# Kernel tuning notes

Hardware: AMD Instinct MI355X
Metric: run time of the kernel (lower is better)

The kernel has to match this reference:

```python
import jax, jax.numpy as jnp
import numpy as np

B, T, D, H = 2, 2048, 1024, 16
HD = D // H
EPS = 1e-5


def setup_inputs() -> dict:
    key = jax.random.key(0)
    ks = jax.random.split(key, 6)
    scale = 0.02
    return {
        "x": jax.random.normal(ks[0], (B, T, D), dtype=jnp.float32),
        "wq": jax.random.normal(ks[1], (D, D), dtype=jnp.float32) * scale,
        "bq": jnp.zeros((D,), dtype=jnp.float32),
        "wk": jax.random.normal(ks[2], (D, D), dtype=jnp.float32) * scale,
        "bk": jnp.zeros((D,), dtype=jnp.float32),
        "wv": jax.random.normal(ks[3], (D, D), dtype=jnp.float32) * scale,
        "bv": jnp.zeros((D,), dtype=jnp.float32),
        "wg": jax.random.normal(ks[4], (D, D), dtype=jnp.float32) * scale,
        "bg": jnp.zeros((D,), dtype=jnp.float32),
        "gamma": jnp.ones((D,), dtype=jnp.float32),
        "beta": jnp.zeros((D,), dtype=jnp.float32),
    }


def reference(x, wq, bq, wk, bk, wv, bv, wg, bg, gamma, beta):
    b, t, d = x.shape
    # projections (torch Linear: y = x @ W^T + b, W stored as (out, in))
    def proj(w, bias):
        return jnp.einsum('btd,ed->bte', x, w) + bias
    q = proj(wq, bq).reshape(b, t, H, HD).swapaxes(1, 2)  # b h t hd
    k = proj(wk, bk).reshape(b, t, H, HD).swapaxes(1, 2)
    v = proj(wv, bv).reshape(b, t, H, HD).swapaxes(1, 2)
    # full (non-causal) attention as in the source
    scores = jnp.einsum('bhqd,bhkd->bhqk', q, k) / jnp.sqrt(jnp.float32(HD))
    attn = jax.nn.softmax(scores, axis=-1)
    out = jnp.einsum('bhqk,bhkd->bhqd', attn, v)
    out = out.swapaxes(1, 2).reshape(b, t, d)  # b t (h hd)
    gate = proj(wg, bg)
    y = gate * out
    # GroupNorm with n_heads groups over the channel (d_model) dim, per token
    yg = y.reshape(b, t, H, HD)
    mu = jnp.mean(yg, axis=-1, keepdims=True)
    var = jnp.var(yg, axis=-1, keepdims=True)
    yn = (yg - mu) / jnp.sqrt(var + EPS)
    yn = yn * gamma.reshape(H, HD) + beta.reshape(H, HD)
    return yn.reshape(b, t, d)
```

## Files before the change

kernel.cpp:

```cpp
#include <hip/hip_runtime.h>
#include <hip/hip_bf16.h>
#include <math.h>

namespace {
constexpr int kB = 2, kT = 2048, kD = 1024, kH = 16, kHD = 64;
}

typedef __attribute__((ext_vector_type(8))) short short8;
typedef __attribute__((ext_vector_type(4))) float f32x4;
typedef __attribute__((ext_vector_type(16))) float f32x16;

#if __has_builtin(__builtin_amdgcn_exp2f)
#define EXP2F(x) __builtin_amdgcn_exp2f(x)
#else
#define EXP2F(x) __expf((x) * 0.6931471805599453f)
#endif

__device__ __forceinline__ ushort f2bf(float f) {
  union { float f; uint u; } c; c.f = f;
  uint u = c.u + 0x7FFFu + ((c.u >> 16) & 1u);
  return (ushort)(u >> 16);
}

__device__ __forceinline__ float bf2f(ushort u) {
  union { uint u; float f; } c; c.u = ((uint)u) << 16; return c.f;
}

__device__ __forceinline__ uint pack_bf2(float a, float b) {
  uint r;
  asm("v_cvt_pk_bf16_f32 %0, %1, %2" : "=v"(r) : "v"(a), "v"(b));
  return r;
}

__device__ __forceinline__ void gload_lds16(const void* g, void* l) {
  __builtin_amdgcn_global_load_lds(
      (const __attribute__((address_space(1))) void*)g,
      (__attribute__((address_space(3))) void*)l, 16, 0, 0);
}

__global__ __launch_bounds__(256) void cvt_kernel(
    const float* __restrict__ x, const float* __restrict__ w0,
    const float* __restrict__ w1, const float* __restrict__ w2,
    const float* __restrict__ w3, ushort* __restrict__ out)
{
  const size_t g = (size_t)blockIdx.x * 256 + threadIdx.x;
  const size_t e = g * 4;
  const float* src; size_t rel;
  if (e < ((size_t)1 << 22)) { src = x; rel = e; }
  else {
    size_t e2 = e - ((size_t)1 << 22);
    int wi = (int)(e2 >> 20);
    src = wi == 0 ? w0 : wi == 1 ? w1 : wi == 2 ? w2 : w3;
    rel = e2 & (((size_t)1 << 20) - 1);
  }
  float4 v = *reinterpret_cast<const float4*>(src + rel);
  ushort4 u;
  u.x = f2bf(v.x); u.y = f2bf(v.y); u.z = f2bf(v.z); u.w = f2bf(v.w);
  *reinterpret_cast<ushort4*>(out + e) = u;
}

__device__ __forceinline__ void stage_half(
    const ushort* __restrict__ src, int row0, int kcol0,
    ushort* ldsbase, int wid, int lane)
{
#pragma unroll
  for (int part = 0; part < 2; ++part) {
    const int c = part * 512 + wid * 64 + lane;
    const int x = c * 16;
    const int o = x ^ (((x >> 7) & 3) << 4);
    const int r = o >> 6;
    const int cb = (o & 63) >> 1;
    gload_lds16(src + (size_t)(row0 + r) * kD + kcol0 + cb, ldsbase + (x >> 1));
  }
}

__device__ __forceinline__ short8 read_frag(const ushort* half, int r, int lg) {
  const int slot = lg ^ ((r >> 1) & 3);
  return *reinterpret_cast<const short8*>(&half[r * 32 + slot * 8]);
}

#define PH_BAR() do { asm volatile("" ::: "memory"); \
  __builtin_amdgcn_s_barrier(); asm volatile("" ::: "memory"); } while (0)

__global__ __launch_bounds__(512, 2) void proj_mfma_kernel(
    const ushort* __restrict__ Xb, const ushort* __restrict__ Wb,
    const float* __restrict__ bq, const float* __restrict__ bk,
    const float* __restrict__ bv, const float* __restrict__ bg,
    ushort* __restrict__ qo, ushort* __restrict__ ko,
    ushort* __restrict__ vt, ushort* __restrict__ go)
{
  const int mat = blockIdx.z;
  const ushort* Wm = Wb + (size_t)mat * 1024 * 1024;
  const float* bias = mat == 0 ? bq : mat == 1 ? bk : mat == 2 ? bv : bg;
  const int m0 = blockIdx.x * 256;
  const int n0g = blockIdx.y * 256;
  const int tid = threadIdx.x;
  const int wid = tid >> 6, lane = tid & 63;
  const int wr = wid >> 2, wc = wid & 3;
  const int wrow = wr * 128, wcol = wc * 64;
  const int lr = lane & 15, lg = lane >> 4;

  __shared__ ushort lds[65536];

  f32x4 acc[8][4];
#pragma unroll
  for (int i = 0; i < 8; ++i)
#pragma unroll
    for (int j = 0; j < 4; ++j) acc[i][j] = (f32x4){0.f, 0.f, 0.f, 0.f};

  short8 bfr[4];

#define STAGE_A(bu, h, kt) stage_half(Xb, m0,  (kt) * 64 + (h) * 32, \
    &lds[(bu) * 32768 + (h) * 8192], wid, lane)
#define STAGE_B(bu, h, kt) stage_half(Wm, n0g, (kt) * 64 + (h) * 32, \
    &lds[(bu) * 32768 + 16384 + (h) * 8192], wid, lane)

#define PHASE(bu, h, MB, READB, STAGE_STMT, DOVM)                          \
  {                                                                        \
    const ushort* Ah = &lds[(bu) * 32768 + (h) * 8192];                    \
    const ushort* Bh = &lds[(bu) * 32768 + 16384 + (h) * 8192];            \
    short8 af[4];                                                          \
    af[0] = read_frag(Ah, wrow + (MB + 0) * 16 + lr, lg);                  \
    af[1] = read_frag(Ah, wrow + (MB + 1) * 16 + lr, lg);                  \
    af[2] = read_frag(Ah, wrow + (MB + 2) * 16 + lr, lg);                  \
    af[3] = read_frag(Ah, wrow + (MB + 3) * 16 + lr, lg);                  \
    if (READB) {                                                           \
      bfr[0] = read_frag(Bh, wcol + 0 * 16 + lr, lg);                      \
      bfr[1] = read_frag(Bh, wcol + 1 * 16 + lr, lg);                      \
      bfr[2] = read_frag(Bh, wcol + 2 * 16 + lr, lg);                      \
      bfr[3] = read_frag(Bh, wcol + 3 * 16 + lr, lg);                      \
    }                                                                      \
    STAGE_STMT;                                                            \
    PH_BAR();                                                              \
    __builtin_amdgcn_s_setprio(1);                                         \
    _Pragma("unroll")                                                      \
    for (int m2 = 0; m2 < 4; ++m2)                                         \
      _Pragma("unroll")                                                    \
      for (int ni = 0; ni < 4; ++ni)                                       \
        acc[(MB) + m2][ni] = __builtin_amdgcn_mfma_f32_16x16x32_bf16(      \
            af[m2], bfr[ni], acc[(MB) + m2][ni], 0, 0, 0);                 \
    __builtin_amdgcn_s_setprio(0);                                         \
    if (DOVM) asm volatile("s_waitcnt vmcnt(4)" ::: "memory");             \
    PH_BAR();                                                              \
  }

  STAGE_A(0, 0, 0); STAGE_B(0, 0, 0);
  STAGE_A(0, 1, 0); STAGE_B(0, 1, 0);
  STAGE_A(1, 0, 1); STAGE_B(1, 0, 1);
  asm volatile("s_waitcnt vmcnt(4)" ::: "memory");
  PH_BAR();

#pragma unroll 1
  for (int it = 0; it < 8; ++it) {
    const int ta = 2 * it, tb = 2 * it + 1;
    const int tn0 = (ta + 2) & 15;
    const int tn1 = (tb + 2) & 15;
    PHASE(0, 0, 0, 1, (STAGE_A(1, 1, tb)),  0)
    PHASE(0, 0, 4, 0, (STAGE_B(1, 1, tb)),  0)
    PHASE(0, 1, 0, 1, (STAGE_A(0, 0, tn0)), 0)
    PHASE(0, 1, 4, 0, (STAGE_B(0, 0, tn0)), 1)
    PHASE(1, 0, 0, 1, (STAGE_A(0, 1, tn0)), 0)
    PHASE(1, 0, 4, 0, (STAGE_B(0, 1, tn0)), 0)
    PHASE(1, 1, 0, 1, (STAGE_A(1, 0, tn1)), 0)
    PHASE(1, 1, 4, 0, (STAGE_B(1, 0, tn1)), 1)
  }

#undef PHASE
#undef STAGE_A
#undef STAGE_B

  const float vsc = (mat == 0) ? 0.18033688f : 1.0f;

#pragma unroll
  for (int mi = 0; mi < 8; ++mi) {
    const int mbase = m0 + wrow + mi * 16 + 4 * lg;
    const int b = mbase >> 11, t0r = mbase & (kT - 1);
#pragma unroll
    for (int ni = 0; ni < 4; ++ni) {
      const int n = n0g + wcol + ni * 16 + lr;
      const float bn = bias[n];
      if (mat == 3) {
#pragma unroll
        for (int r = 0; r < 4; ++r)
          go[(size_t)(mbase + r) * kD + n] = f2bf(acc[mi][ni][r] + bn);
      } else if (mat == 2) {
        const int h = n >> 6, hd = n & 63;
        const int bh = b * kH + h;
        const int nh = hd >> 5, lv = hd & 31;
        const int kc = t0r >> 5, kk0 = t0r & 31;
        const int jf = kk0 >> 4, hi2 = (kk0 >> 3) & 1, jj0 = kk0 & 7;
        const int lane2 = lv + hi2 * 32;
        const size_t off =
            (((((size_t)bh * 64 + kc) * 2 + nh) * 2 + jf) * 64 + lane2) * 8 + jj0;
        ushort4 u;
        u.x = f2bf(acc[mi][ni][0] + bn); u.y = f2bf(acc[mi][ni][1] + bn);
        u.z = f2bf(acc[mi][ni][2] + bn); u.w = f2bf(acc[mi][ni][3] + bn);
        *reinterpret_cast<ushort4*>(&vt[off]) = u;
      } else {
        const int h = n >> 6, hd = n & 63;
        const int bh = b * kH + h;
        const int hk = hd >> 4, hi2 = (hd >> 3) & 1, jj = hd & 7;
        ushort* dst = (mat == 0) ? qo : ko;
#pragma unroll
        for (int r = 0; r < 4; ++r) {
          const int t = t0r + r;
          const int kc = t >> 5, kk = t & 31;
          const size_t off =
              ((((size_t)bh * 64 + kc) * 4 + hk) * 64 + kk + hi2 * 32) * 8 + jj;
          dst[off] = f2bf((acc[mi][ni][r] + bn) * vsc);
        }
      }
    }
  }
}

__global__ __launch_bounds__(256, 4) void attn_mfma32_kernel(
    const ushort* __restrict__ Qf, const ushort* __restrict__ Kf,
    const ushort* __restrict__ Vf, ushort* __restrict__ Op,
    float* __restrict__ lsumP)
{
  const int bid = blockIdx.x;
  const int xcd = bid & 7;
  const int j = bid >> 3;
  const int bh = xcd * 4 + (j >> 6);
  const int rem = j & 63;
  const int qt = rem & 15;
  const int ks = rem >> 4;
  const int tid = threadIdx.x, w = tid >> 6, lane = tid & 63;
  const int lq = lane & 31;
  const int hi = lane >> 5;

  const ushort* qfp = Qf + (((size_t)bh * 64 + (qt * 4 + w)) * 4) * 512;
  short8 aq[4];
#pragma unroll
  for (int hk = 0; hk < 4; ++hk)
    aq[hk] = *reinterpret_cast<const short8*>(&qfp[((size_t)hk * 64 + lane) * 8]);

  f32x16 oacc[2];
#pragma unroll
  for (int nh = 0; nh < 2; ++nh)
#pragma unroll
    for (int r = 0; r < 16; ++r) oacc[nh][r] = 0.f;
  float lsum = 0.f;

  const ushort* kfp = Kf + ((size_t)bh * 64 + ks * 16) * 2048;
  const ushort* vfp = Vf + ((size_t)bh * 64 + ks * 16) * 2048;

  for (int kt = 0; kt < 16; ++kt) {
    short8 kf_[4];
#pragma unroll
    for (int hk = 0; hk < 4; ++hk)
      kf_[hk] = *reinterpret_cast<const short8*>(&kfp[((size_t)hk * 64 + lane) * 8]);
    kfp += 2048;

    short8 vf[2][2];
#pragma unroll
    for (int nh = 0; nh < 2; ++nh)
#pragma unroll
      for (int jf = 0; jf < 2; ++jf)
        vf[nh][jf] = *reinterpret_cast<const short8*>(
            &vfp[(((size_t)nh * 2 + jf) * 64 + lane) * 8]);
    vfp += 2048;

    f32x16 s;
#pragma unroll
    for (int r = 0; r < 16; ++r) s[r] = 0.f;
    __builtin_amdgcn_s_setprio(1);
#pragma unroll
    for (int hk = 0; hk < 4; ++hk)
      s = __builtin_amdgcn_mfma_f32_32x32x16_bf16(kf_[hk], aq[hk], s, 0, 0, 0);
    __builtin_amdgcn_s_setprio(0);

    float p[16];
#pragma unroll
    for (int r = 0; r < 16; ++r) p[r] = EXP2F(s[r]);
    float t0 = 0.f, t1 = 0.f;
#pragma unroll
    for (int r = 0; r < 16; r += 2) { t0 += p[r]; t1 += p[r + 1]; }
    lsum += t0 + t1;

    uint pk[8];
#pragma unroll
    for (int m = 0; m < 8; ++m) pk[m] = pack_bf2(p[2 * m], p[2 * m + 1]);

    union { uint u[4]; short8 s8; } fa0, fa1;
#if __has_builtin(__builtin_amdgcn_permlane32_swap)
    {
      auto s0 = __builtin_amdgcn_permlane32_swap(pk[0], pk[2], false, false);
      auto s1 = __builtin_amdgcn_permlane32_swap(pk[1], pk[3], false, false);
      auto s2 = __builtin_amdgcn_permlane32_swap(pk[4], pk[6], false, false);
      auto s3 = __builtin_amdgcn_permlane32_swap(pk[5], pk[7], false, false);
      fa0.u[0] = s0[0]; fa0.u[2] = s0[1];
      fa0.u[1] = s1[0]; fa0.u[3] = s1[1];
      fa1.u[0] = s2[0]; fa1.u[2] = s2[1];
      fa1.u[1] = s3[0]; fa1.u[3] = s3[1];
    }
#else
    {
      const uint x0 = hi ? pk[0] : pk[2];
      const uint x1 = hi ? pk[1] : pk[3];
      const uint x2 = hi ? pk[4] : pk[6];
      const uint x3 = hi ? pk[5] : pk[7];
      const uint r0 = __shfl_xor((int)x0, 32);
      const uint r1 = __shfl_xor((int)x1, 32);
      const uint r2 = __shfl_xor((int)x2, 32);
      const uint r3 = __shfl_xor((int)x3, 32);
      if (hi == 0) {
        fa0.u[0] = pk[0]; fa0.u[1] = pk[1]; fa0.u[2] = r0; fa0.u[3] = r1;
        fa1.u[0] = pk[4]; fa1.u[1] = pk[5]; fa1.u[2] = r2; fa1.u[3] = r3;
      } else {
        fa0.u[0] = r0; fa0.u[1] = r1; fa0.u[2] = pk[2]; fa0.u[3] = pk[3];
        fa1.u[0] = r2; fa1.u[1] = r3; fa1.u[2] = pk[6]; fa1.u[3] = pk[7];
      }
    }
#endif

    __builtin_amdgcn_s_setprio(1);
    oacc[0] = __builtin_amdgcn_mfma_f32_32x32x16_bf16(vf[0][0], fa0.s8, oacc[0], 0, 0, 0);
    oacc[0] = __builtin_amdgcn_mfma_f32_32x32x16_bf16(vf[0][1], fa1.s8, oacc[0], 0, 0, 0);
    oacc[1] = __builtin_amdgcn_mfma_f32_32x32x16_bf16(vf[1][0], fa0.s8, oacc[1], 0, 0, 0);
    oacc[1] = __builtin_amdgcn_mfma_f32_32x32x16_bf16(vf[1][1], fa1.s8, oacc[1], 0, 0, 0);
    __builtin_amdgcn_s_setprio(0);
  }

  lsum += __shfl_xor(lsum, 32);

  const int q0 = qt * 128 + w * 32;
  const size_t prow = (((size_t)ks * 32 + bh) * kT + (q0 + lq)) * kHD;
#pragma unroll
  for (int nh = 0; nh < 2; ++nh)
#pragma unroll
    for (int g2 = 0; g2 < 4; ++g2) {
      ushort4 u;
      u.x = f2bf(oacc[nh][4 * g2 + 0]);
      u.y = f2bf(oacc[nh][4 * g2 + 1]);
      u.z = f2bf(oacc[nh][4 * g2 + 2]);
      u.w = f2bf(oacc[nh][4 * g2 + 3]);
      *reinterpret_cast<ushort4*>(&Op[prow + nh * 32 + 8 * g2 + 4 * hi]) = u;
    }
  if (hi == 0)
    lsumP[((size_t)ks * 32 + bh) * kT + q0 + lq] = lsum;
}

__global__ __launch_bounds__(256) void gn_kernel(
    const ushort* __restrict__ gb, const ushort* __restrict__ Op,
    const float* __restrict__ lsumP,
    const float* __restrict__ gamma, const float* __restrict__ beta,
    float* __restrict__ out)
{
  const int grp = blockIdx.x * 4 + (threadIdx.x >> 6);
  const int lane = threadIdx.x & 63;
  const int bt = grp >> 4, h = grp & 15;
  const int b = bt >> 11, t = bt & (kT - 1);
  const int bh = b * kH + h;

  float o_un = 0.f, l = 0.f;
#pragma unroll
  for (int ks = 0; ks < 4; ++ks) {
    const size_t base = ((size_t)ks * 32 + bh) * kT + t;
    o_un += bf2f(Op[base * kHD + lane]);
    l += lsumP[base];
  }
  const float o = o_un / l;
  const float y = bf2f(gb[(size_t)bt * kD + h * kHD + lane]) * o;

  float s = y, ss = y * y;
#pragma unroll
  for (int off = 32; off; off >>= 1) {
    s  += __shfl_xor(s, off);
    ss += __shfl_xor(ss, off);
  }
  const float mean = s * (1.f / 64.f);
  const float var  = ss * (1.f / 64.f) - mean * mean;
  const float inv  = rsqrtf(var + 1e-5f);
  out[(size_t)bt * kD + h * kHD + lane] =
      (y - mean) * inv * gamma[h * kHD + lane] + beta[h * kHD + lane];
}

extern "C" void kernel_launch(void* const* d_in, const int* in_sizes, int n_in,
                              void* d_out, int out_size, void* d_ws, size_t ws_size,
                              hipStream_t stream) {
  const float* x     = (const float*)d_in[0];
  const float* wq    = (const float*)d_in[1];
  const float* bq    = (const float*)d_in[2];
  const float* wk    = (const float*)d_in[3];
  const float* bk    = (const float*)d_in[4];
  const float* wv    = (const float*)d_in[5];
  const float* bv    = (const float*)d_in[6];
  const float* wg    = (const float*)d_in[7];
  const float* bg    = (const float*)d_in[8];
  const float* gamma = (const float*)d_in[9];
  const float* beta  = (const float*)d_in[10];

  ushort* cb  = (ushort*)d_ws;
  ushort* qb  = cb + (size_t)8388608;
  ushort* kb  = qb + (size_t)4194304;
  ushort* vtb = kb + (size_t)4194304;
  ushort* gb  = vtb + (size_t)4194304;
  ushort* Op  = gb + (size_t)4194304;
  float*  lsumP = (float*)cb;
  float*  out = (float*)d_out;

  const ushort* xb = cb;
  const ushort* wb = cb + (size_t)4194304;

  cvt_kernel<<<8192, 256, 0, stream>>>(x, wq, wk, wv, wg, cb);
  proj_mfma_kernel<<<dim3(16, 4, 4), 512, 0, stream>>>(
      xb, wb, bq, bk, bv, bg, qb, kb, vtb, gb);
  attn_mfma32_kernel<<<2048, 256, 0, stream>>>(qb, kb, vtb, Op, lsumP);
  gn_kernel<<<16384, 256, 0, stream>>>(gb, Op, lsumP, gamma, beta, out);
}
```

Before: 114.1 us.

## Stage K/V tiles through double-buffered LDS with direct global-to-LDS loads

The attention kernel no longer has each wave read K and V fragments straight from global memory. The block now loads each K/V tile into shared memory once, using direct global-to-LDS loads into two alternating buffers, so the next tile's load overlaps the current tile's MFMA and exp work. This removes the redundant per-wave global reads of the same tile, at the cost of 16 KB of LDS per block and two block-wide barriers per pair of tiles. It also drops the shuffle fallback for the permlane32 swap, and its correctness depends on the barrier waiting for the asynchronous LDS loads to complete.

New measurement: 109.9 us. 3.7% less time.

```diff
diff --git a/kernel.cpp b/kernel.cpp
--- a/kernel.cpp
+++ b/kernel.cpp
@@ -230,6 +230,9 @@
   const int lq = lane & 31;
   const int hi = lane >> 5;
 
+  __shared__ ushort kvA[4096];
+  __shared__ ushort kvB[4096];
+
   const ushort* qfp = Qf + (((size_t)bh * 64 + (qt * 4 + w)) * 4) * 512;
   short8 aq[4];
 #pragma unroll
@@ -243,85 +246,78 @@
     for (int r = 0; r < 16; ++r) oacc[nh][r] = 0.f;
   float lsum = 0.f;
 
-  const ushort* kfp = Kf + ((size_t)bh * 64 + ks * 16) * 2048;
-  const ushort* vfp = Vf + ((size_t)bh * 64 + ks * 16) * 2048;
-
-  for (int kt = 0; kt < 16; ++kt) {
-    short8 kf_[4];
-#pragma unroll
-    for (int hk = 0; hk < 4; ++hk)
-      kf_[hk] = *reinterpret_cast<const short8*>(&kfp[((size_t)hk * 64 + lane) * 8]);
-    kfp += 2048;
-
-    short8 vf[2][2];
-#pragma unroll
-    for (int nh = 0; nh < 2; ++nh)
-#pragma unroll
-      for (int jf = 0; jf < 2; ++jf)
-        vf[nh][jf] = *reinterpret_cast<const short8*>(
-            &vfp[(((size_t)nh * 2 + jf) * 64 + lane) * 8]);
-    vfp += 2048;
-
-    f32x16 s;
-#pragma unroll
-    for (int r = 0; r < 16; ++r) s[r] = 0.f;
-    __builtin_amdgcn_s_setprio(1);
-#pragma unroll
-    for (int hk = 0; hk < 4; ++hk)
-      s = __builtin_amdgcn_mfma_f32_32x32x16_bf16(kf_[hk], aq[hk], s, 0, 0, 0);
-    __builtin_amdgcn_s_setprio(0);
-
-    float p[16];
-#pragma unroll
-    for (int r = 0; r < 16; ++r) p[r] = EXP2F(s[r]);
-    float t0 = 0.f, t1 = 0.f;
-#pragma unroll
-    for (int r = 0; r < 16; r += 2) { t0 += p[r]; t1 += p[r + 1]; }
-    lsum += t0 + t1;
-
-    uint pk[8];
-#pragma unroll
-    for (int m = 0; m < 8; ++m) pk[m] = pack_bf2(p[2 * m], p[2 * m + 1]);
-
-    union { uint u[4]; short8 s8; } fa0, fa1;
-#if __has_builtin(__builtin_amdgcn_permlane32_swap)
-    {
-      auto s0 = __builtin_amdgcn_permlane32_swap(pk[0], pk[2], false, false);
-      auto s1 = __builtin_amdgcn_permlane32_swap(pk[1], pk[3], false, false);
-      auto s2 = __builtin_amdgcn_permlane32_swap(pk[4], pk[6], false, false);
-      auto s3 = __builtin_amdgcn_permlane32_swap(pk[5], pk[7], false, false);
-      fa0.u[0] = s0[0]; fa0.u[2] = s0[1];
-      fa0.u[1] = s1[0]; fa0.u[3] = s1[1];
-      fa1.u[0] = s2[0]; fa1.u[2] = s2[1];
-      fa1.u[1] = s3[0]; fa1.u[3] = s3[1];
-    }
-#else
-    {
-      const uint x0 = hi ? pk[0] : pk[2];
-      const uint x1 = hi ? pk[1] : pk[3];
-      const uint x2 = hi ? pk[4] : pk[6];
-      const uint x3 = hi ? pk[5] : pk[7];
-      const uint r0 = __shfl_xor((int)x0, 32);
-      const uint r1 = __shfl_xor((int)x1, 32);
-      const uint r2 = __shfl_xor((int)x2, 32);
-      const uint r3 = __shfl_xor((int)x3, 32);
-      if (hi == 0) {
-        fa0.u[0] = pk[0]; fa0.u[1] = pk[1]; fa0.u[2] = r0; fa0.u[3] = r1;
-        fa1.u[0] = pk[4]; fa1.u[1] = pk[5]; fa1.u[2] = r2; fa1.u[3] = r3;
-      } else {
-        fa0.u[0] = r0; fa0.u[1] = r1; fa0.u[2] = pk[2]; fa0.u[3] = pk[3];
-        fa1.u[0] = r2; fa1.u[1] = r3; fa1.u[2] = pk[6]; fa1.u[3] = pk[7];
-      }
-    }
-#endif
-
-    __builtin_amdgcn_s_setprio(1);
-    oacc[0] = __builtin_amdgcn_mfma_f32_32x32x16_bf16(vf[0][0], fa0.s8, oacc[0], 0, 0, 0);
-    oacc[0] = __builtin_amdgcn_mfma_f32_32x32x16_bf16(vf[0][1], fa1.s8, oacc[0], 0, 0, 0);
-    oacc[1] = __builtin_amdgcn_mfma_f32_32x32x16_bf16(vf[1][0], fa0.s8, oacc[1], 0, 0, 0);
-    oacc[1] = __builtin_amdgcn_mfma_f32_32x32x16_bf16(vf[1][1], fa1.s8, oacc[1], 0, 0, 0);
-    __builtin_amdgcn_s_setprio(0);
-  }
+  const ushort* kbase = Kf + ((size_t)bh * 64 + ks * 16) * 2048;
+  const ushort* vbase = Vf + ((size_t)bh * 64 + ks * 16) * 2048;
+
+#define STAGE_KV(dst, t) do {                                               \
+    gload_lds16(kbase + (size_t)(t) * 2048 + tid * 8, &dst[tid * 8]);       \
+    gload_lds16(vbase + (size_t)(t) * 2048 + tid * 8, &dst[2048 + tid * 8]);\
+  } while (0)
+
+#define COMPUTE_KV(buf) do {                                                \
+    short8 kf_[4];                                                          \
+    _Pragma("unroll")                                                       \
+    for (int hk = 0; hk < 4; ++hk)                                          \
+      kf_[hk] = *reinterpret_cast<const short8*>(&buf[(hk * 64 + lane) * 8]);\
+    short8 vf[2][2];                                                        \
+    _Pragma("unroll")                                                       \
+    for (int nh = 0; nh < 2; ++nh)                                          \
+      _Pragma("unroll")                                                     \
+      for (int jf = 0; jf < 2; ++jf)                                        \
+        vf[nh][jf] = *reinterpret_cast<const short8*>(                      \
+            &buf[2048 + ((nh * 2 + jf) * 64 + lane) * 8]);                  \
+    f32x16 s;                                                               \
+    _Pragma("unroll")                                                       \
+    for (int r = 0; r < 16; ++r) s[r] = 0.f;                                \
+    __builtin_amdgcn_s_setprio(1);                                          \
+    _Pragma("unroll")                                                       \
+    for (int hk = 0; hk < 4; ++hk)                                          \
+      s = __builtin_amdgcn_mfma_f32_32x32x16_bf16(kf_[hk], aq[hk], s, 0, 0, 0);\
+    __builtin_amdgcn_s_setprio(0);                                          \
+    float p[16];                                                            \
+    _Pragma("unroll")                                                       \
+    for (int r = 0; r < 16; ++r) p[r] = EXP2F(s[r]);                        \
+    float t0 = 0.f, t1 = 0.f;                                               \
+    _Pragma("unroll")                                                       \
+    for (int r = 0; r < 16; r += 2) { t0 += p[r]; t1 += p[r + 1]; }         \
+    lsum += t0 + t1;                                                        \
+    uint pk[8];                                                             \
+    _Pragma("unroll")                                                       \
+    for (int m = 0; m < 8; ++m) pk[m] = pack_bf2(p[2 * m], p[2 * m + 1]);   \
+    union { uint u[4]; short8 s8; } fa0, fa1;                               \
+    {                                                                       \
+      auto s0 = __builtin_amdgcn_permlane32_swap(pk[0], pk[2], false, false);\
+      auto s1 = __builtin_amdgcn_permlane32_swap(pk[1], pk[3], false, false);\
+      auto s2 = __builtin_amdgcn_permlane32_swap(pk[4], pk[6], false, false);\
+      auto s3 = __builtin_amdgcn_permlane32_swap(pk[5], pk[7], false, false);\
+      fa0.u[0] = s0[0]; fa0.u[2] = s0[1];                                   \
+      fa0.u[1] = s1[0]; fa0.u[3] = s1[1];                                   \
+      fa1.u[0] = s2[0]; fa1.u[2] = s2[1];                                   \
+      fa1.u[1] = s3[0]; fa1.u[3] = s3[1];                                   \
+    }                                                                       \
+    __builtin_amdgcn_s_setprio(1);                                          \
+    oacc[0] = __builtin_amdgcn_mfma_f32_32x32x16_bf16(vf[0][0], fa0.s8, oacc[0], 0, 0, 0);\
+    oacc[0] = __builtin_amdgcn_mfma_f32_32x32x16_bf16(vf[0][1], fa1.s8, oacc[0], 0, 0, 0);\
+    oacc[1] = __builtin_amdgcn_mfma_f32_32x32x16_bf16(vf[1][0], fa0.s8, oacc[1], 0, 0, 0);\
+    oacc[1] = __builtin_amdgcn_mfma_f32_32x32x16_bf16(vf[1][1], fa1.s8, oacc[1], 0, 0, 0);\
+    __builtin_amdgcn_s_setprio(0);                                          \
+  } while (0)
+
+  STAGE_KV(kvA, 0);
+  __syncthreads();
+
+#pragma unroll 1
+  for (int kt = 0; kt < 16; kt += 2) {
+    if (kt + 1 < 16) STAGE_KV(kvB, kt + 1);
+    COMPUTE_KV(kvA);
+    __syncthreads();
+    if (kt + 2 < 16) STAGE_KV(kvA, kt + 2);
+    COMPUTE_KV(kvB);
+    __syncthreads();
+  }
+
+#undef STAGE_KV
+#undef COMPUTE_KV
 
   lsum += __shfl_xor(lsum, 32);
 
```
